# Kernel optimization log

Hardware: AMD Instinct MI355X
Metric: run time of the kernel (lower is better)

The kernel has to match this reference:

```python
import jax, jax.numpy as jnp
import numpy as np

N_HEADS = 16
EMBD = 1024
D_HEAD = EMBD // N_HEADS

def setup_inputs() -> dict:
    key = jax.random.key(0)
    ks = jax.random.split(key, 5)
    x = jax.random.normal(ks[0], (2, 2048, EMBD), dtype=jnp.float32)
    # Linear weights stored torch-style [out, in]; apply as x @ W.T + b
    W_in = jax.random.normal(ks[1], (3 * EMBD, EMBD), dtype=jnp.float32) * (EMBD ** -0.5)
    b_in = jax.random.normal(ks[2], (3 * EMBD,), dtype=jnp.float32) * 0.01
    W_out = jax.random.normal(ks[3], (EMBD, EMBD), dtype=jnp.float32) * (EMBD ** -0.5)
    b_out = jax.random.normal(ks[4], (EMBD,), dtype=jnp.float32) * 0.01
    return {"x": x, "W_in": W_in, "b_in": b_in, "W_out": W_out, "b_out": b_out}

def reference(x, W_in, b_in, W_out, b_out):
    B, S, D = x.shape
    qkv = x @ W_in.T + b_in                      # [B, S, 3D]
    q, k, v = jnp.split(qkv, 3, axis=-1)
    def heads(t):
        return t.reshape(B, S, N_HEADS, D_HEAD).transpose(0, 2, 1, 3)  # [B,H,S,d]
    q, k, v = heads(q), heads(k), heads(v)
    scale = 1.0 / jnp.sqrt(jnp.float32(D_HEAD))
    scores = jnp.einsum('bhqd,bhkd->bhqk', q, k) * scale
    weights = jax.nn.softmax(scores, axis=-1)
    out = jnp.einsum('bhqk,bhkd->bhqd', weights, v)  # [B,H,S,d]
    out = out.transpose(0, 2, 1, 3).reshape(B, S, D)
    return out @ W_out.T + b_out
```

## Files before the change

kernel.cpp:

```cpp
#include <hip/hip_runtime.h>
#include <cstdint>

#define EMBD 1024
#define NH 16
#define DH 64
#define BB 2
#define SS 2048
#define M_TOT (BB*SS)
#define N_QKV (3*EMBD)

typedef __bf16 bf16_t;
typedef bf16_t bf16x8 __attribute__((ext_vector_type(8)));
typedef float f32x4 __attribute__((ext_vector_type(4)));
typedef unsigned short u16;
typedef unsigned int u32;

static __device__ __forceinline__ u16 f2bf(float f) {
    union { float f; unsigned u; } c; c.f = f;
    unsigned u = c.u;
    unsigned r = (u + 0x7FFFu + ((u >> 16) & 1u)) >> 16;
    return (u16)r;
}

#define GLDS16(gp, lp) \
    __builtin_amdgcn_global_load_lds((const __attribute__((address_space(1))) void*)(gp), \
                                     (__attribute__((address_space(3))) void*)(lp), 16, 0, 0)

#define NX8 (M_TOT * EMBD / 8)
#define NWI8 (N_QKV * EMBD / 8)
#define NWO8 (EMBD * EMBD / 8)
__global__ void cast_all(const float* __restrict__ x, const float* __restrict__ wi,
                         const float* __restrict__ wo, u16* __restrict__ xb,
                         u16* __restrict__ wib, u16* __restrict__ wob) {
    int i = blockIdx.x * blockDim.x + threadIdx.x;
    const float* s; u16* d; int off;
    if (i < NX8)              { s = x;  d = xb;  off = i; }
    else if (i < NX8 + NWI8)  { s = wi; d = wib; off = i - NX8; }
    else                      { s = wo; d = wob; off = i - NX8 - NWI8; }
    const float4* s4 = (const float4*)s;
    float4 a = s4[2 * off];
    float4 b = s4[2 * off + 1];
    union { u16 u[8]; uint4 v; } r;
    r.u[0] = f2bf(a.x); r.u[1] = f2bf(a.y); r.u[2] = f2bf(a.z); r.u[3] = f2bf(a.w);
    r.u[4] = f2bf(b.x); r.u[5] = f2bf(b.y); r.u[6] = f2bf(b.z); r.u[7] = f2bf(b.w);
    ((uint4*)d)[off] = r.v;
}

#define QSCALE (0.125f * 1.4426950408889634f)
__global__ __launch_bounds__(256) void gemm_qkv(
    const u16* __restrict__ Xb,
    const u16* __restrict__ Wb,
    const float* __restrict__ b_in,
    u16* __restrict__ Q, u16* __restrict__ Kf, u16* __restrict__ Vpf)
{
    __shared__ u16 AB[3][8192];
    const int t = threadIdx.x;
    const int lane = t & 63;
    const int wave = t >> 6;
    const int wm = wave >> 1, wn = wave & 1;
    const int quad = lane >> 4, l16 = lane & 15;
    const int m0 = blockIdx.y * 128, n0 = blockIdx.x * 128;

    const int s0i = t, s1i = 256 + t;
    const u16* ga0 = Xb + (size_t)(m0 + (s0i >> 2)) * EMBD + (s0i & 3) * 8;
    const u16* ga1 = Xb + (size_t)(m0 + (s1i >> 2)) * EMBD + (s1i & 3) * 8;
    const u16* gb0 = Wb + (size_t)(n0 + (s0i >> 2)) * EMBD + (s0i & 3) * 8;
    const u16* gb1 = Wb + (size_t)(n0 + (s1i >> 2)) * EMBD + (s1i & 3) * 8;

    f32x4 acc[4][4] = {};

#pragma unroll
    for (int p = 0; p < 2; ++p) {
        u16* buf = &AB[p][0];
        GLDS16(ga0 + p * 32, buf + s0i * 8);
        GLDS16(ga1 + p * 32, buf + s1i * 8);
        GLDS16(gb0 + p * 32, buf + 4096 + s0i * 8);
        GLDS16(gb1 + p * 32, buf + 4096 + s1i * 8);
    }

    int bi = 0;
    int bw = 2;
    for (int it = 0; it < EMBD / 32; ++it) {
        asm volatile("s_waitcnt vmcnt(4)" ::: "memory");
        __syncthreads();
        {
            int k0 = (it + 2) * 32;
            u16* buf = &AB[bw][0];
            GLDS16(ga0 + k0, buf + s0i * 8);
            GLDS16(ga1 + k0, buf + s1i * 8);
            GLDS16(gb0 + k0, buf + 4096 + s0i * 8);
            GLDS16(gb1 + k0, buf + 4096 + s1i * 8);
        }
        const u16* As = &AB[bi][0];
        const u16* Bs = &AB[bi][4096];
        bf16x8 af[4], bfr[4];
#pragma unroll
        for (int im = 0; im < 4; ++im)
            af[im] = *(const bf16x8*)(As + (wm * 64 + im * 16 + l16) * 32 + quad * 8);
#pragma unroll
        for (int in = 0; in < 4; ++in)
            bfr[in] = *(const bf16x8*)(Bs + (wn * 64 + in * 16 + l16) * 32 + quad * 8);
#pragma unroll
        for (int im = 0; im < 4; ++im)
#pragma unroll
            for (int in = 0; in < 4; ++in)
                acc[im][in] = __builtin_amdgcn_mfma_f32_16x16x32_bf16(
                    af[im], bfr[in], acc[im][in], 0, 0, 0);
        bi = (bi == 2) ? 0 : bi + 1;
        bw = (bw == 2) ? 0 : bw + 1;
    }

#pragma unroll
    for (int im = 0; im < 4; ++im) {
        int rbase = m0 + wm * 64 + im * 16 + quad * 4;
        int b = rbase >> 11, ss = rbase & (SS - 1);
#pragma unroll
        for (int in = 0; in < 4; ++in) {
            int col = n0 + wn * 64 + in * 16 + l16;
            float bias = b_in[col];
            float v0 = acc[im][in][0] + bias;
            float v1 = acc[im][in][1] + bias;
            float v2 = acc[im][in][2] + bias;
            float v3 = acc[im][in][3] + bias;
            if (col < EMBD) {
                int h = col >> 6, d = col & 63;
                u16* qp = Q + (((size_t)(b * NH + h) * SS) + ss) * DH + d;
                qp[0]      = f2bf(v0 * QSCALE);
                qp[DH]     = f2bf(v1 * QSCALE);
                qp[2 * DH] = f2bf(v2 * QSCALE);
                qp[3 * DH] = f2bf(v3 * QSCALE);
            } else if (col < 2 * EMBD) {
                int c = col - EMBD; int h = c >> 6, d = c & 63;
                int qf = (d >> 3) & 3;
                int sA = (ss >> 1) & 3;
                int sB = (sA + 1) & 3;
                u16* kp = Kf + (size_t)(b * NH + h) * SS * DH
                          + (ss >> 4) * 1024 + (d >> 5) * 512
                          + (ss & 15) * 32 + (d & 7);
                kp[(qf ^ sA) * 8]      = f2bf(v0);
                kp[32 + (qf ^ sA) * 8] = f2bf(v1);
                kp[64 + (qf ^ sB) * 8] = f2bf(v2);
                kp[96 + (qf ^ sB) * 8] = f2bf(v3);
            } else {
                int c = col - 2 * EMBD; int h = c >> 6, d = c & 63;
                int p32 = ((((ss >> 2) & 3) ^ ((d >> 1) & 3)) * 8)
                          + ((ss >> 4) & 1) * 4;
                u32 lo = (u32)f2bf(v0) | ((u32)f2bf(v1) << 16);
                u32 hi = (u32)f2bf(v2) | ((u32)f2bf(v3) << 16);
                uint2 pk; pk.x = lo; pk.y = hi;
                *(uint2*)(Vpf + (size_t)(b * NH + h) * SS * DH
                          + (ss >> 5) * 2048 + (d >> 4) * 512 + (d & 15) * 32 + p32) = pk;
            }
        }
    }
}

#define OST 72
__global__ __launch_bounds__(256, 2) void attn(
    const u16* __restrict__ Q, const u16* __restrict__ Kf,
    const u16* __restrict__ Vpf, u16* __restrict__ AO)
{
    __shared__ u16 KV[2][16384];
    const int t = threadIdx.x;
    const int lane = t & 63, w = t >> 6;
    const int quad = lane >> 4, l16 = lane & 15;
    const int sq8 = (quad ^ ((l16 >> 1) & 3)) * 8;
    const int b0 = blockIdx.x;
    const int bh = (b0 & 7) * 4 + ((b0 >> 3) & 3);
    const int qt = b0 >> 5;
    const int q0 = qt * 128 + w * 32;

    const u16* Qh = Q + ((size_t)bh * SS + q0) * DH;
    const u16* Kh = Kf + (size_t)bh * SS * DH;
    const u16* Vh = Vpf + (size_t)bh * SS * DH;

    bf16x8 qb[2][2];
#pragma unroll
    for (int qi = 0; qi < 2; ++qi) {
        qb[qi][0] = *(const bf16x8*)(Qh + (qi * 16 + l16) * DH + quad * 8);
        qb[qi][1] = *(const bf16x8*)(Qh + (qi * 16 + l16) * DH + 32 + quad * 8);
    }

    f32x4 o[2][4] = {};
    float lsum[2] = {0.f, 0.f};

#pragma unroll
    for (int i = 0; i < 4; ++i) {
        GLDS16(Kh + i * 2048 + t * 8, &KV[0][0] + i * 2048 + t * 8);
        GLDS16(Vh + i * 2048 + t * 8, &KV[0][8192] + i * 2048 + t * 8);
    }

    for (int it = 0; it < SS / 128; ++it) {
        asm volatile("s_waitcnt vmcnt(0)" ::: "memory");
        __syncthreads();
        if (it + 1 < SS / 128) {
            const u16* kc = Kh + (it + 1) * 8192;
            const u16* vc = Vh + (it + 1) * 8192;
            u16* kb = &KV[(it + 1) & 1][0];
            u16* vb = &KV[(it + 1) & 1][8192];
#pragma unroll
            for (int i = 0; i < 4; ++i) {
                GLDS16(kc + i * 2048 + t * 8, kb + i * 2048 + t * 8);
                GLDS16(vc + i * 2048 + t * 8, vb + i * 2048 + t * 8);
            }
        }
        const u16* Kb = &KV[it & 1][0];
        const u16* Vb = &KV[it & 1][8192];
#pragma unroll
        for (int g = 0; g < 4; ++g) {
            bf16x8 ka00 = *(const bf16x8*)(Kb + (2 * g) * 1024 +       l16 * 32 + sq8);
            bf16x8 ka01 = *(const bf16x8*)(Kb + (2 * g) * 1024 + 512 + l16 * 32 + sq8);
            bf16x8 ka10 = *(const bf16x8*)(Kb + (2 * g + 1) * 1024 +       l16 * 32 + sq8);
            bf16x8 ka11 = *(const bf16x8*)(Kb + (2 * g + 1) * 1024 + 512 + l16 * 32 + sq8);
            bf16x8 va0 = *(const bf16x8*)(Vb + g * 2048 +        l16 * 32 + sq8);
            bf16x8 va1 = *(const bf16x8*)(Vb + g * 2048 + 512  + l16 * 32 + sq8);
            bf16x8 va2 = *(const bf16x8*)(Vb + g * 2048 + 1024 + l16 * 32 + sq8);
            bf16x8 va3 = *(const bf16x8*)(Vb + g * 2048 + 1536 + l16 * 32 + sq8);
            bf16x8 pb[2];
#pragma unroll
            for (int qi = 0; qi < 2; ++qi) {
                f32x4 z0 = {0.f, 0.f, 0.f, 0.f};
                f32x4 z1 = {0.f, 0.f, 0.f, 0.f};
                __builtin_amdgcn_s_setprio(1);
                z0 = __builtin_amdgcn_mfma_f32_16x16x32_bf16(ka00, qb[qi][0], z0, 0, 0, 0);
                z0 = __builtin_amdgcn_mfma_f32_16x16x32_bf16(ka01, qb[qi][1], z0, 0, 0, 0);
                z1 = __builtin_amdgcn_mfma_f32_16x16x32_bf16(ka10, qb[qi][0], z1, 0, 0, 0);
                z1 = __builtin_amdgcn_mfma_f32_16x16x32_bf16(ka11, qb[qi][1], z1, 0, 0, 0);
                __builtin_amdgcn_s_setprio(0);
                u32 ue[8];
                float ls = 0.f;
#pragma unroll
                for (int j = 0; j < 4; ++j) {
                    float e0 = __builtin_amdgcn_exp2f(z0[j]);
                    float e1 = __builtin_amdgcn_exp2f(z1[j]);
                    ls += e0 + e1;
                    union { float f; u32 v; } c0, c1;
                    c0.f = e0; c1.f = e1;
                    ue[j] = c0.v + 0x8000u;
                    ue[4 + j] = c1.v + 0x8000u;
                }
                lsum[qi] += ls;
                union { uint4 u; bf16x8 b; } cv;
                cv.u.x = __builtin_amdgcn_perm(ue[1], ue[0], 0x07060302u);
                cv.u.y = __builtin_amdgcn_perm(ue[3], ue[2], 0x07060302u);
                cv.u.z = __builtin_amdgcn_perm(ue[5], ue[4], 0x07060302u);
                cv.u.w = __builtin_amdgcn_perm(ue[7], ue[6], 0x07060302u);
                pb[qi] = cv.b;
            }
            __builtin_amdgcn_s_setprio(1);
            o[0][0] = __builtin_amdgcn_mfma_f32_16x16x32_bf16(va0, pb[0], o[0][0], 0, 0, 0);
            o[0][1] = __builtin_amdgcn_mfma_f32_16x16x32_bf16(va1, pb[0], o[0][1], 0, 0, 0);
            o[0][2] = __builtin_amdgcn_mfma_f32_16x16x32_bf16(va2, pb[0], o[0][2], 0, 0, 0);
            o[0][3] = __builtin_amdgcn_mfma_f32_16x16x32_bf16(va3, pb[0], o[0][3], 0, 0, 0);
            o[1][0] = __builtin_amdgcn_mfma_f32_16x16x32_bf16(va0, pb[1], o[1][0], 0, 0, 0);
            o[1][1] = __builtin_amdgcn_mfma_f32_16x16x32_bf16(va1, pb[1], o[1][1], 0, 0, 0);
            o[1][2] = __builtin_amdgcn_mfma_f32_16x16x32_bf16(va2, pb[1], o[1][2], 0, 0, 0);
            o[1][3] = __builtin_amdgcn_mfma_f32_16x16x32_bf16(va3, pb[1], o[1][3], 0, 0, 0);
            __builtin_amdgcn_s_setprio(0);
        }
    }

    float rl[2];
#pragma unroll
    for (int qi = 0; qi < 2; ++qi) {
        float v = lsum[qi];
        v += __shfl_xor(v, 16, 64);
        v += __shfl_xor(v, 32, 64);
        rl[qi] = 1.0f / v;
    }
    __syncthreads();
    u16* Ksc = &KV[0][0];
#pragma unroll
    for (int qi = 0; qi < 2; ++qi)
#pragma unroll
        for (int dt = 0; dt < 4; ++dt)
#pragma unroll
            for (int jj = 0; jj < 2; ++jj) {
                u32 lo_ = (u32)f2bf(o[qi][dt][2 * jj] * rl[qi]);
                u32 hi_ = (u32)f2bf(o[qi][dt][2 * jj + 1] * rl[qi]);
                *(u32*)(Ksc + (w * 32 + qi * 16 + l16) * OST + dt * 16 + quad * 4 + jj * 2) =
                    lo_ | (hi_ << 16);
            }
    __syncthreads();
    const int b = bh >> 4, h = bh & 15;
#pragma unroll
    for (int i = 0; i < 4; ++i) {
        int idx = i * 256 + t;
        int q = idx >> 3, c = idx & 7;
        uint4 vv = *(const uint4*)(Ksc + q * OST + c * 8);
        *(uint4*)(AO + ((size_t)(b * SS + qt * 128 + q)) * EMBD + h * DH + c * 8) = vv;
    }
}

__global__ __launch_bounds__(256) void gemm_out(
    const u16* __restrict__ Ab,
    const u16* __restrict__ Wb,
    const float* __restrict__ b_out,
    float* __restrict__ Out)
{
    __shared__ u16 AB[3][8192];
    const int t = threadIdx.x;
    const int lane = t & 63;
    const int wave = t >> 6;
    const int wm = wave >> 1, wn = wave & 1;
    const int quad = lane >> 4, l16 = lane & 15;
    const int m0 = blockIdx.y * 128, n0 = blockIdx.x * 128;

    const int s0i = t, s1i = 256 + t;
    const u16* ga0 = Ab + (size_t)(m0 + (s0i >> 2)) * EMBD + (s0i & 3) * 8;
    const u16* ga1 = Ab + (size_t)(m0 + (s1i >> 2)) * EMBD + (s1i & 3) * 8;
    const u16* gb0 = Wb + (size_t)(n0 + (s0i >> 2)) * EMBD + (s0i & 3) * 8;
    const u16* gb1 = Wb + (size_t)(n0 + (s1i >> 2)) * EMBD + (s1i & 3) * 8;

    f32x4 acc[4][4] = {};

#pragma unroll
    for (int p = 0; p < 2; ++p) {
        u16* buf = &AB[p][0];
        GLDS16(ga0 + p * 32, buf + s0i * 8);
        GLDS16(ga1 + p * 32, buf + s1i * 8);
        GLDS16(gb0 + p * 32, buf + 4096 + s0i * 8);
        GLDS16(gb1 + p * 32, buf + 4096 + s1i * 8);
    }

    int bi = 0, bw = 2;
    for (int it = 0; it < EMBD / 32; ++it) {
        asm volatile("s_waitcnt vmcnt(4)" ::: "memory");
        __syncthreads();
        {
            int k0 = (it + 2) * 32;
            u16* buf = &AB[bw][0];
            GLDS16(ga0 + k0, buf + s0i * 8);
            GLDS16(ga1 + k0, buf + s1i * 8);
            GLDS16(gb0 + k0, buf + 4096 + s0i * 8);
            GLDS16(gb1 + k0, buf + 4096 + s1i * 8);
        }
        const u16* As = &AB[bi][0];
        const u16* Bs = &AB[bi][4096];
        bf16x8 af[4], bfr[4];
#pragma unroll
        for (int im = 0; im < 4; ++im)
            af[im] = *(const bf16x8*)(As + (wm * 64 + im * 16 + l16) * 32 + quad * 8);
#pragma unroll
        for (int in = 0; in < 4; ++in)
            bfr[in] = *(const bf16x8*)(Bs + (wn * 64 + in * 16 + l16) * 32 + quad * 8);
#pragma unroll
        for (int im = 0; im < 4; ++im)
#pragma unroll
            for (int in = 0; in < 4; ++in)
                acc[im][in] = __builtin_amdgcn_mfma_f32_16x16x32_bf16(
                    af[im], bfr[in], acc[im][in], 0, 0, 0);
        bi = (bi == 2) ? 0 : bi + 1;
        bw = (bw == 2) ? 0 : bw + 1;
    }

#pragma unroll
    for (int im = 0; im < 4; ++im) {
        int rbase = m0 + wm * 64 + im * 16 + quad * 4;
#pragma unroll
        for (int in = 0; in < 4; ++in) {
            int col = n0 + wn * 64 + in * 16 + l16;
            float bias = b_out[col];
#pragma unroll
            for (int j = 0; j < 4; ++j)
                Out[(size_t)(rbase + j) * EMBD + col] = acc[im][in][j] + bias;
        }
    }
}

extern "C" void kernel_launch(void* const* d_in, const int* in_sizes, int n_in,
                              void* d_out, int out_size, void* d_ws, size_t ws_size,
                              hipStream_t stream)
{
    (void)in_sizes; (void)n_in; (void)out_size; (void)ws_size;
    const float* x     = (const float*)d_in[0];
    const float* W_in  = (const float*)d_in[1];
    const float* b_in  = (const float*)d_in[2];
    const float* W_out = (const float*)d_in[3];
    const float* b_out = (const float*)d_in[4];
    float* out = (float*)d_out;

    char* ws = (char*)d_ws;
    u16* xb  = (u16*)(ws);
    u16* wib = (u16*)(ws + 8u  * 1024 * 1024);
    u16* wob = (u16*)(ws + 14u * 1024 * 1024);
    u16* Qw  = (u16*)(ws + 16u * 1024 * 1024);
    u16* Kw  = (u16*)(ws + 24u * 1024 * 1024);
    u16* Vpw = (u16*)(ws + 32u * 1024 * 1024);
    u16* AO  = (u16*)(ws + 40u * 1024 * 1024);

    cast_all<<<(NX8 + NWI8 + NWO8) / 256, 256, 0, stream>>>(x, W_in, W_out, xb, wib, wob);
    gemm_qkv<<<dim3(N_QKV / 128, M_TOT / 128), 256, 0, stream>>>(xb, wib, b_in, Qw, Kw, Vpw);
    attn<<<512, 256, 0, stream>>>(Qw, Kw, Vpw, AO);
    gemm_out<<<dim3(EMBD / 128, M_TOT / 128), 256, 0, stream>>>(AO, wob, b_out, out);
}
```

Before: 180.0 us.

## Triple-buffer attention KV chunks, compute row sums via MFMA, retile output GEMM

The attention kernel switches from double-buffered 128-key chunks to triple-buffered 64-key chunks, so loads for chunk it+2 overlap compute and the wait is relaxed to vmcnt(4). The softmax denominator is no longer summed with VALU adds and cross-lane shuffles; an extra MFMA against a ones vector accumulates it. The output GEMM tile shrinks from 128x128 to 128x64, doubling the block count to improve CU occupancy on a small GEMM, at the cost of less operand reuse per block. The extra MFMAs add matrix-unit work, and the per-iteration barriers double.

```diff
diff --git a/kernel.cpp b/kernel.cpp
--- a/kernel.cpp
+++ b/kernel.cpp
@@ -156,11 +156,12 @@
 }
 
 #define OST 72
+#define NCH (SS / 64)
 __global__ __launch_bounds__(256, 2) void attn(
     const u16* __restrict__ Q, const u16* __restrict__ Kf,
     const u16* __restrict__ Vpf, u16* __restrict__ AO)
 {
-    __shared__ u16 KV[2][16384];
+    __shared__ u16 KV[3][8192];
     const int t = threadIdx.x;
     const int lane = t & 63, w = t >> 6;
     const int quad = lane >> 4, l16 = lane & 15;
@@ -181,33 +182,40 @@
         qb[qi][1] = *(const bf16x8*)(Qh + (qi * 16 + l16) * DH + 32 + quad * 8);
     }
 
+    union { u16 u[8]; bf16x8 b; } onesu;
+#pragma unroll
+    for (int j = 0; j < 8; ++j) onesu.u[j] = 0x3F80u;
+    const bf16x8 ones = onesu.b;
+
     f32x4 o[2][4] = {};
-    float lsum[2] = {0.f, 0.f};
-
-#pragma unroll
-    for (int i = 0; i < 4; ++i) {
-        GLDS16(Kh + i * 2048 + t * 8, &KV[0][0] + i * 2048 + t * 8);
-        GLDS16(Vh + i * 2048 + t * 8, &KV[0][8192] + i * 2048 + t * 8);
-    }
-
-    for (int it = 0; it < SS / 128; ++it) {
-        asm volatile("s_waitcnt vmcnt(0)" ::: "memory");
+    f32x4 ol[2] = {};
+
+#pragma unroll
+    for (int p = 0; p < 2; ++p) {
+        GLDS16(Kh + p * 4096 + t * 8,        &KV[p][0] + t * 8);
+        GLDS16(Kh + p * 4096 + 2048 + t * 8, &KV[p][0] + 2048 + t * 8);
+        GLDS16(Vh + p * 4096 + t * 8,        &KV[p][4096] + t * 8);
+        GLDS16(Vh + p * 4096 + 2048 + t * 8, &KV[p][4096] + 2048 + t * 8);
+    }
+
+    int bi = 0, bw = 2;
+    for (int it = 0; it < NCH; ++it) {
+        asm volatile("s_waitcnt vmcnt(4)" ::: "memory");
         __syncthreads();
-        if (it + 1 < SS / 128) {
-            const u16* kc = Kh + (it + 1) * 8192;
-            const u16* vc = Vh + (it + 1) * 8192;
-            u16* kb = &KV[(it + 1) & 1][0];
-            u16* vb = &KV[(it + 1) & 1][8192];
-#pragma unroll
-            for (int i = 0; i < 4; ++i) {
-                GLDS16(kc + i * 2048 + t * 8, kb + i * 2048 + t * 8);
-                GLDS16(vc + i * 2048 + t * 8, vb + i * 2048 + t * 8);
-            }
-        }
-        const u16* Kb = &KV[it & 1][0];
-        const u16* Vb = &KV[it & 1][8192];
-#pragma unroll
-        for (int g = 0; g < 4; ++g) {
+        if (it < NCH - 1) {
+            const u16* kc = Kh + (it + 2) * 4096;
+            const u16* vc = Vh + (it + 2) * 4096;
+            u16* kb = &KV[bw][0];
+            u16* vb = &KV[bw][4096];
+            GLDS16(kc + t * 8,        kb + t * 8);
+            GLDS16(kc + 2048 + t * 8, kb + 2048 + t * 8);
+            GLDS16(vc + t * 8,        vb + t * 8);
+            GLDS16(vc + 2048 + t * 8, vb + 2048 + t * 8);
+        }
+        const u16* Kb = &KV[bi][0];
+        const u16* Vb = &KV[bi][4096];
+#pragma unroll
+        for (int g = 0; g < 2; ++g) {
             bf16x8 ka00 = *(const bf16x8*)(Kb + (2 * g) * 1024 +       l16 * 32 + sq8);
             bf16x8 ka01 = *(const bf16x8*)(Kb + (2 * g) * 1024 + 512 + l16 * 32 + sq8);
             bf16x8 ka10 = *(const bf16x8*)(Kb + (2 * g + 1) * 1024 +       l16 * 32 + sq8);
@@ -228,18 +236,15 @@
                 z1 = __builtin_amdgcn_mfma_f32_16x16x32_bf16(ka11, qb[qi][1], z1, 0, 0, 0);
                 __builtin_amdgcn_s_setprio(0);
                 u32 ue[8];
-                float ls = 0.f;
 #pragma unroll
                 for (int j = 0; j < 4; ++j) {
                     float e0 = __builtin_amdgcn_exp2f(z0[j]);
                     float e1 = __builtin_amdgcn_exp2f(z1[j]);
-                    ls += e0 + e1;
                     union { float f; u32 v; } c0, c1;
                     c0.f = e0; c1.f = e1;
                     ue[j] = c0.v + 0x8000u;
                     ue[4 + j] = c1.v + 0x8000u;
                 }
-                lsum[qi] += ls;
                 union { uint4 u; bf16x8 b; } cv;
                 cv.u.x = __builtin_amdgcn_perm(ue[1], ue[0], 0x07060302u);
                 cv.u.y = __builtin_amdgcn_perm(ue[3], ue[2], 0x07060302u);
@@ -252,22 +257,21 @@
             o[0][1] = __builtin_amdgcn_mfma_f32_16x16x32_bf16(va1, pb[0], o[0][1], 0, 0, 0);
             o[0][2] = __builtin_amdgcn_mfma_f32_16x16x32_bf16(va2, pb[0], o[0][2], 0, 0, 0);
             o[0][3] = __builtin_amdgcn_mfma_f32_16x16x32_bf16(va3, pb[0], o[0][3], 0, 0, 0);
+            ol[0]   = __builtin_amdgcn_mfma_f32_16x16x32_bf16(ones, pb[0], ol[0], 0, 0, 0);
             o[1][0] = __builtin_amdgcn_mfma_f32_16x16x32_bf16(va0, pb[1], o[1][0], 0, 0, 0);
             o[1][1] = __builtin_amdgcn_mfma_f32_16x16x32_bf16(va1, pb[1], o[1][1], 0, 0, 0);
             o[1][2] = __builtin_amdgcn_mfma_f32_16x16x32_bf16(va2, pb[1], o[1][2], 0, 0, 0);
             o[1][3] = __builtin_amdgcn_mfma_f32_16x16x32_bf16(va3, pb[1], o[1][3], 0, 0, 0);
+            ol[1]   = __builtin_amdgcn_mfma_f32_16x16x32_bf16(ones, pb[1], ol[1], 0, 0, 0);
             __builtin_amdgcn_s_setprio(0);
         }
+        bi = (bi == 2) ? 0 : bi + 1;
+        bw = (bw == 2) ? 0 : bw + 1;
     }
 
     float rl[2];
-#pragma unroll
-    for (int qi = 0; qi < 2; ++qi) {
-        float v = lsum[qi];
-        v += __shfl_xor(v, 16, 64);
-        v += __shfl_xor(v, 32, 64);
-        rl[qi] = 1.0f / v;
-    }
+    rl[0] = 1.0f / ol[0][0];
+    rl[1] = 1.0f / ol[1][0];
     __syncthreads();
     u16* Ksc = &KV[0][0];
 #pragma unroll
@@ -298,54 +302,49 @@
     const float* __restrict__ b_out,
     float* __restrict__ Out)
 {
-    __shared__ u16 AB[3][8192];
+    __shared__ u16 AB[3][6144];
     const int t = threadIdx.x;
     const int lane = t & 63;
     const int wave = t >> 6;
-    const int wm = wave >> 1, wn = wave & 1;
     const int quad = lane >> 4, l16 = lane & 15;
-    const int m0 = blockIdx.y * 128, n0 = blockIdx.x * 128;
-
-    const int s0i = t, s1i = 256 + t;
-    const u16* ga0 = Ab + (size_t)(m0 + (s0i >> 2)) * EMBD + (s0i & 3) * 8;
-    const u16* ga1 = Ab + (size_t)(m0 + (s1i >> 2)) * EMBD + (s1i & 3) * 8;
-    const u16* gb0 = Wb + (size_t)(n0 + (s0i >> 2)) * EMBD + (s0i & 3) * 8;
-    const u16* gb1 = Wb + (size_t)(n0 + (s1i >> 2)) * EMBD + (s1i & 3) * 8;
-
-    f32x4 acc[4][4] = {};
+    const int m0 = blockIdx.y * 128, n0 = blockIdx.x * 64;
+
+    const u16* ga0 = Ab + (size_t)(m0 + (t >> 2)) * EMBD + (t & 3) * 8;
+    const u16* ga1 = Ab + (size_t)(m0 + 64 + (t >> 2)) * EMBD + (t & 3) * 8;
+    const u16* gb0 = Wb + (size_t)(n0 + (t >> 2)) * EMBD + (t & 3) * 8;
+
+    f32x4 acc[2][4] = {};
 
 #pragma unroll
     for (int p = 0; p < 2; ++p) {
         u16* buf = &AB[p][0];
-        GLDS16(ga0 + p * 32, buf + s0i * 8);
-        GLDS16(ga1 + p * 32, buf + s1i * 8);
-        GLDS16(gb0 + p * 32, buf + 4096 + s0i * 8);
-        GLDS16(gb1 + p * 32, buf + 4096 + s1i * 8);
+        GLDS16(ga0 + p * 32, buf + t * 8);
+        GLDS16(ga1 + p * 32, buf + 2048 + t * 8);
+        GLDS16(gb0 + p * 32, buf + 4096 + t * 8);
     }
 
     int bi = 0, bw = 2;
     for (int it = 0; it < EMBD / 32; ++it) {
-        asm volatile("s_waitcnt vmcnt(4)" ::: "memory");
+        asm volatile("s_waitcnt vmcnt(3)" ::: "memory");
         __syncthreads();
         {
             int k0 = (it + 2) * 32;
             u16* buf = &AB[bw][0];
-            GLDS16(ga0 + k0, buf + s0i * 8);
-            GLDS16(ga1 + k0, buf + s1i * 8);
-            GLDS16(gb0 + k0, buf + 4096 + s0i * 8);
-            GLDS16(gb1 + k0, buf + 4096 + s1i * 8);
+            GLDS16(ga0 + k0, buf + t * 8);
+            GLDS16(ga1 + k0, buf + 2048 + t * 8);
+            GLDS16(gb0 + k0, buf + 4096 + t * 8);
         }
         const u16* As = &AB[bi][0];
         const u16* Bs = &AB[bi][4096];
-        bf16x8 af[4], bfr[4];
-#pragma unroll
-        for (int im = 0; im < 4; ++im)
-            af[im] = *(const bf16x8*)(As + (wm * 64 + im * 16 + l16) * 32 + quad * 8);
+        bf16x8 af[2], bfr[4];
+#pragma unroll
+        for (int im = 0; im < 2; ++im)
+            af[im] = *(const bf16x8*)(As + (wave * 32 + im * 16 + l16) * 32 + quad * 8);
 #pragma unroll
         for (int in = 0; in < 4; ++in)
-            bfr[in] = *(const bf16x8*)(Bs + (wn * 64 + in * 16 + l16) * 32 + quad * 8);
-#pragma unroll
-        for (int im = 0; im < 4; ++im)
+            bfr[in] = *(const bf16x8*)(Bs + (in * 16 + l16) * 32 + quad * 8);
+#pragma unroll
+        for (int im = 0; im < 2; ++im)
 #pragma unroll
             for (int in = 0; in < 4; ++in)
                 acc[im][in] = __builtin_amdgcn_mfma_f32_16x16x32_bf16(
@@ -355,11 +354,11 @@
     }
 
 #pragma unroll
-    for (int im = 0; im < 4; ++im) {
-        int rbase = m0 + wm * 64 + im * 16 + quad * 4;
+    for (int im = 0; im < 2; ++im) {
+        int rbase = m0 + wave * 32 + im * 16 + quad * 4;
 #pragma unroll
         for (int in = 0; in < 4; ++in) {
-            int col = n0 + wn * 64 + in * 16 + l16;
+            int col = n0 + in * 16 + l16;
             float bias = b_out[col];
 #pragma unroll
             for (int j = 0; j < 4; ++j)
@@ -392,5 +391,5 @@
     cast_all<<<(NX8 + NWI8 + NWO8) / 256, 256, 0, stream>>>(x, W_in, W_out, xb, wib, wob);
     gemm_qkv<<<dim3(N_QKV / 128, M_TOT / 128), 256, 0, stream>>>(xb, wib, b_in, Qw, Kw, Vpw);
     attn<<<512, 256, 0, stream>>>(Qw, Kw, Vpw, AO);
-    gemm_out<<<dim3(EMBD / 128, M_TOT / 128), 256, 0, stream>>>(AO, wob, b_out, out);
-}
+    gemm_out<<<dim3(EMBD / 64, M_TOT / 128), 256, 0, stream>>>(AO, wob, b_out, out);
+}
```

Measured after the change: 176.9 us. Within noise of the previous version (-1.7%).
